# Performance work log

Measured on AMD Instinct MI355X. Metric: run time of the kernel, lower is better.

## Reference

```python
import jax, jax.numpy as jnp
import numpy as np

NUM_BINS_X = 512
NUM_BINS_Y = 512
XL, YL, XH, YH = 0.0, 0.0, 1.0, 1.0
ROUTING_H = 50000.0
ROUTING_V = 50000.0
MACRO_UTIL_H = 10.0
MACRO_UTIL_V = 10.0
NUM_NETS = 131072
PINS_PER_NET = 4
NUM_MOVABLE = 50000
NUM_TERMINALS = 5000
NUM_NODES = NUM_MOVABLE + NUM_TERMINALS
NUM_PINS = NUM_NETS * PINS_PER_NET
BIN_SIZE_X = (XH - XL) / NUM_BINS_X
BIN_SIZE_Y = (YH - YL) / NUM_BINS_Y


def setup_inputs():
    key = jax.random.key(0)
    k1, k2, k3, k4 = jax.random.split(key, 4)
    # pin_pos = [x_0..x_P-1, y_0..y_P-1], pos = [x_0..x_N-1, y_0..y_N-1]
    pin_pos = jax.random.uniform(k1, (2 * NUM_PINS,), dtype=jnp.float32, minval=XL, maxval=XH)
    pos = jax.random.uniform(k2, (2 * NUM_NODES,), dtype=jnp.float32, minval=XL, maxval=0.9 * (XH - XL))
    node_size_x = jax.random.uniform(k3, (NUM_NODES,), dtype=jnp.float32, minval=0.01, maxval=0.05)
    node_size_y = jax.random.uniform(k4, (NUM_NODES,), dtype=jnp.float32, minval=0.01, maxval=0.05)
    net_weights = jnp.ones((NUM_NETS,), jnp.float32)
    rng = np.random.default_rng(0)
    flat_netpin = jnp.asarray(rng.permutation(NUM_PINS).astype(np.int32))
    movable = rng.choice(NUM_MOVABLE, 64, replace=False)
    fixed = NUM_MOVABLE + rng.choice(NUM_TERMINALS, 32, replace=False)
    macro_indexes = jnp.asarray(np.concatenate([movable, fixed]).astype(np.int32))
    return dict(pos=pos, pin_pos=pin_pos, node_size_x=node_size_x, node_size_y=node_size_y,
                net_weights=net_weights, flat_netpin=flat_netpin, macro_indexes=macro_indexes)


def _bin_overlap(lo, hi, origin, bin_size, num_bins):
    # [N, num_bins]: overlap length of interval [lo, hi] with each bin along one axis
    edges = origin + bin_size * jnp.arange(num_bins, dtype=lo.dtype)
    return jnp.clip(jnp.minimum(hi[:, None], edges[None, :] + bin_size)
                    - jnp.maximum(lo[:, None], edges[None, :]), 0.0, None)


def _blur3(m, sigma):
    # torchvision GaussianBlur(kernel_size=3, sigma), separable, reflect padding
    x = jnp.array([-1.0, 0.0, 1.0], m.dtype)
    k = jnp.exp(-0.5 * (x / sigma) ** 2)
    k = k / k.sum()
    mp = jnp.pad(m, ((1, 1), (0, 0)), mode='reflect')
    m = k[0] * mp[:-2] + k[1] * mp[1:-1] + k[2] * mp[2:]
    mp = jnp.pad(m, ((0, 0), (1, 1)), mode='reflect')
    return k[0] * mp[:, :-2] + k[1] * mp[:, 1:-1] + k[2] * mp[:, 2:]


def _rudy_maps(pos, pin_pos, node_size_x, node_size_y, net_weights, flat_netpin, macro_indexes):
    # net bounding boxes from pins (fixed PINS_PER_NET pins per net)
    px = pin_pos[:NUM_PINS][flat_netpin].reshape(NUM_NETS, PINS_PER_NET)
    py = pin_pos[NUM_PINS:][flat_netpin].reshape(NUM_NETS, PINS_PER_NET)
    x_min, x_max = px.min(1), px.max(1)
    y_min, y_max = py.min(1), py.max(1)
    ox = _bin_overlap(x_min, x_max, XL, BIN_SIZE_X, NUM_BINS_X)   # [N, Bx]
    oy = _bin_overlap(y_min, y_max, YL, BIN_SIZE_Y, NUM_BINS_Y)   # [N, By]
    wh = net_weights / (y_max - y_min)  # RUDY horizontal demand density
    wv = net_weights / (x_max - x_min)  # RUDY vertical demand density
    H = jnp.einsum('nx,ny->xy', ox * wh[:, None], oy)
    V = jnp.einsum('nx,ny->xy', ox * wv[:, None], oy)
    # macro contributions
    mx = pos[macro_indexes]
    my = pos[NUM_NODES + macro_indexes]
    msx = node_size_x[macro_indexes]
    msy = node_size_y[macro_indexes]
    area = msx * msy
    mox = _bin_overlap(mx, mx + msx, XL, BIN_SIZE_X, NUM_BINS_X)
    moy = _bin_overlap(my, my + msy, YL, BIN_SIZE_Y, NUM_BINS_Y)
    H = H + jnp.einsum('mx,my->xy', mox * (MACRO_UTIL_H / area)[:, None], moy)
    V = V + jnp.einsum('mx,my->xy', mox * (MACRO_UTIL_V / area)[:, None], moy)
    num_bins = NUM_BINS_X * NUM_BINS_Y
    H = H / (ROUTING_H / num_bins)
    V = V / (ROUTING_V / num_bins)
    sigma = min((XH - XL) / BIN_SIZE_X, (YH - YL) / BIN_SIZE_Y) / 16.0
    return _blur3(H, sigma), _blur3(V, sigma)


def reference(pos, pin_pos, node_size_x, node_size_y, net_weights, flat_netpin, macro_indexes):
    H, V = _rudy_maps(pos, pin_pos, node_size_x, node_size_y, net_weights, flat_netpin, macro_indexes)
    h_ov = jnp.maximum(H - 1.0, 0.0)
    v_ov = jnp.maximum(V - 1.0, 0.0)
    h_cnt = (h_ov > 0).sum()
    v_cnt = (v_ov > 0).sum()
    total_overflow = h_cnt + v_cnt          # total overflow bin area
    max_overflow = jnp.maximum(h_cnt, v_cnt)  # jit-compatible proxy for largest contour area
    route_utilization_map = jnp.maximum(jnp.abs(H), jnp.abs(V))
    return route_utilization_map, max_overflow, total_overflow
```

## Files before the change

kernel.cpp:

```cpp
#include <hip/hip_runtime.h>

#define N_NETS  131072
#define N_PINS  (N_NETS * 4)
#define N_NODES 55000
#define NBBLK   129
#define NPARTS  4
#define CELLCAP 128

__device__ uint4 g_ent[64 * NBBLK * CELLCAP * 2];
__device__ unsigned short g_cellcnt[64 * NBBLK];
__device__ float g_part[NPARTS * 512 * 1024];
__device__ int      g_cnt2[2];
__device__ unsigned g_tick;

__global__ __launch_bounds__(1024) void k_bbox(
    const float* __restrict__ pos, const float* __restrict__ pin_pos,
    const float* __restrict__ nsx, const float* __restrict__ nsy,
    const float* __restrict__ nw,  const int* __restrict__ fnp,
    const int* __restrict__ mid, int nm)
{
    __shared__ int s_cnt[64];
    int tid = threadIdx.x;
    int b = blockIdx.x;
    int t = b * 1024 + tid;
    if (b == 0 && tid == 0) { g_cnt2[0] = 0; g_cnt2[1] = 0; g_tick = 0; }
    if (tid < 64) s_cnt[tid] = 0;
    __syncthreads();

    if (t < N_NETS + nm) {
        float xmin, xmax, ymin, ymax, wh, wv;
        if (t < N_NETS) {
            int4 p = ((const int4*)fnp)[t];
            float x0 = pin_pos[p.x], x1 = pin_pos[p.y], x2 = pin_pos[p.z], x3 = pin_pos[p.w];
            float y0 = pin_pos[N_PINS + p.x], y1 = pin_pos[N_PINS + p.y];
            float y2 = pin_pos[N_PINS + p.z], y3 = pin_pos[N_PINS + p.w];
            xmin = fminf(fminf(x0, x1), fminf(x2, x3));
            xmax = fmaxf(fmaxf(x0, x1), fmaxf(x2, x3));
            ymin = fminf(fminf(y0, y1), fminf(y2, y3));
            ymax = fmaxf(fmaxf(y0, y1), fmaxf(y2, y3));
            float w = nw[t];
            wh = w / (ymax - ymin);
            wv = w / (xmax - xmin);
        } else {
            int idx = mid[t - N_NETS];
            xmin = pos[idx]; ymin = pos[N_NODES + idx];
            float sx = nsx[idx], sy = nsy[idx];
            xmax = xmin + sx; ymax = ymin + sy;
            wh = wv = 10.0f / (sx * sy);
        }
        const float B = 1.0f / 512.0f;
        int xl = min(max((int)(xmin * 512.0f), 0), 511);
        int xh = min(max((int)(xmax * 512.0f), 0), 511);
        int yl = min(max((int)(ymin * 512.0f), 0), 511);
        int yh = min(max((int)(ymax * 512.0f), 0), 511);
        unsigned w0c = (unsigned)yl | ((unsigned)(yl + 1) << 16);
        unsigned w1c = (unsigned)yh | ((unsigned)(yh + 1) << 16);
        float4 pys = make_float4((yl + 1) * B - ymin, ymin - yl * B,
                                 ymax - (yh + 1) * B, yh * B - ymax);
        uint4 Bq = make_uint4(__float_as_uint(pys.x), __float_as_uint(pys.y),
                              __float_as_uint(pys.z), __float_as_uint(pys.w));

        auto put = [&](int row, float px) {
            int s = row & 63;
            int slot = atomicAdd(&s_cnt[s], 1);
            if (slot < CELLCAP) {
                uint4 A;
                A.x = w0c | ((unsigned)(row >> 6) << 29);
                A.y = w1c;
                A.z = __float_as_uint(px * wh);
                A.w = __float_as_uint(px * wv);
                unsigned base = ((unsigned)(s * NBBLK + b) * CELLCAP + (unsigned)slot) * 2u;
                g_ent[base]     = A;
                g_ent[base + 1] = Bq;
            }
        };
        put(xl, (xl + 1) * B - xmin);
        if (xl + 1 < 512) put(xl + 1, xmin - xl * B);
        put(xh, xmax - (xh + 1) * B);
        if (xh + 1 < 512) put(xh + 1, xh * B - xmax);
    }
    __syncthreads();
    if (tid < 64) g_cellcnt[tid * NBBLK + b] = (unsigned short)min(s_cnt[tid], CELLCAP);
}

__global__ __launch_bounds__(1024) void k_deposit() {
    __shared__ float tile[8706];
    __shared__ int s_pref[64];
    __shared__ int s_total;
    int tid = threadIdx.x;
    int s = blockIdx.x >> 2, p = blockIdx.x & 3;
#pragma unroll
    for (int k = tid; k < 8706; k += 1024) tile[k] = 0.0f;

    int lob = (NBBLK * p) >> 2, hib = (NBBLK * (p + 1)) >> 2;
    int nb = hib - lob;
    if (tid < 64) {
        int c = (tid < nb) ? (int)g_cellcnt[s * NBBLK + lob + tid] : 0;
        int v = c;
#pragma unroll
        for (int off = 1; off < 64; off <<= 1) {
            int tv = __shfl_up(v, off);
            if (tid >= off) v += tv;
        }
        s_pref[tid] = v - c;
        if (tid == 63) s_total = v;
    }
    __syncthreads();

    int total = s_total;
    for (int k = tid; k < total; k += 1024) {
        int loJ = 0, hiJ = 63;
#pragma unroll
        for (int st = 0; st < 6; ++st) {
            int mid_ = (loJ + hiJ + 1) >> 1;
            if (s_pref[mid_] <= k) loJ = mid_; else hiJ = mid_ - 1;
        }
        unsigned gidx = ((unsigned)(s * NBBLK + lob + loJ) * CELLCAP
                         + (unsigned)(k - s_pref[loJ])) * 2u;
        uint4 A  = g_ent[gidx];
        uint4 Bq = g_ent[gidx + 1];
        int rr = (int)(A.x >> 29);
        unsigned c0 = A.x & 0xFFFFu, c1 = (A.x >> 16) & 0x1FFFu;
        unsigned c2 = A.y & 0xFFFFu, c3 = A.y >> 16;
        float ah = __uint_as_float(A.z), av = __uint_as_float(A.w);
        float p0 = __uint_as_float(Bq.x), p1 = __uint_as_float(Bq.y);
        float p2 = __uint_as_float(Bq.z), p3 = __uint_as_float(Bq.w);
        int base = rr * 1024;
        int i0 = (c0 < 512u) ? base + 2 * (int)c0 : 8192;
        int i1 = (c1 < 512u) ? base + 2 * (int)c1 : 8192;
        int i2 = (c2 < 512u) ? base + 2 * (int)c2 : 8192;
        int i3 = (c3 < 512u) ? base + 2 * (int)c3 : 8192;
        unsafeAtomicAdd(&tile[i0],     ah * p0);
        unsafeAtomicAdd(&tile[i0 + 1], av * p0);
        unsafeAtomicAdd(&tile[i1],     ah * p1);
        unsafeAtomicAdd(&tile[i1 + 1], av * p1);
        unsafeAtomicAdd(&tile[i2],     ah * p2);
        unsafeAtomicAdd(&tile[i2 + 1], av * p2);
        unsafeAtomicAdd(&tile[i3],     ah * p3);
        unsafeAtomicAdd(&tile[i3 + 1], av * p3);
    }
    __syncthreads();

    int wid = tid >> 6, lane = tid & 63;
    if (wid < 8) {
        float2* rowp = (float2*)&tile[wid * 1024];
        float cx = 0.0f, cy = 0.0f;
        for (int ch = 0; ch < 8; ++ch) {
            float2 v = rowp[ch * 64 + lane];
#pragma unroll
            for (int off = 1; off < 64; off <<= 1) {
                float tx = __shfl_up(v.x, off);
                float ty = __shfl_up(v.y, off);
                if (lane >= off) { v.x += tx; v.y += ty; }
            }
            v.x += cx; v.y += cy;
            rowp[ch * 64 + lane] = v;
            cx = __shfl(v.x, 63); cy = __shfl(v.y, 63);
        }
    }
    __syncthreads();
    int dstp = p * 524288 + (s << 10);
#pragma unroll
    for (int k = 0; k < 8; ++k) {
        int idx = tid + k * 1024;
        int rr = idx >> 10, cc = idx & 1023;
        g_part[dstp + (rr << 16) + cc] = tile[idx];
    }
}

__global__ __launch_bounds__(1024) void k_finish(float* __restrict__ out) {
    __shared__ float sB[16 * 512];
    int tid = threadIdx.x;
    int b = blockIdx.x;
    int lane = tid & 63;
    int c20 = tid & 31;
    int xg = tid >> 5;
    int jj = (c20 < 10) ? c20 : c20 - 10;
    int cy = 8 * b - 1 + jj;
    if (cy < 0) cy = 1;
    if (cy > 511) cy = 510;
    int map = (c20 < 10) ? 0 : 1;
    int gcol = 2 * cy + map;
    const float kw  = expf(-0.5f / 1024.0f);
    const float k1n = 1.0f / (1.0f + 2.0f * kw);
    const float k0n = kw * k1n;
    const float scale = 262144.0f / 50000.0f;
    bool active = c20 < 20;
    int t8  = (c20 < 10) ? c20 - 1 : c20 - 11;

    for (int xo = 0; xo < 16; ++xo) {
        int x = xo * 32 + xg;
        float v = 0.0f;
        if (active) {
            int base = x * 1024 + gcol;
#pragma unroll
            for (int p = 0; p < NPARTS; ++p) v += g_part[p * 524288 + base];
        }
        float vm = __shfl(v, lane - 1);
        float vp = __shfl(v, lane + 1);
        float yb = (k0n * (vm + vp) + k1n * v) * scale;
        if (t8 >= 0 && t8 < 8) sB[(map * 8 + t8) * 512 + x] = yb;
    }
    __syncthreads();

    int w = tid >> 6;
    float s0,s1,s2,s3,s4,s5,s6,s7;
    {
        float4 a  = *(float4*)&sB[w * 512 + lane * 8];
        float4 bq = *(float4*)&sB[w * 512 + lane * 8 + 4];
        s0 = a.x; s1 = s0 + a.y; s2 = s1 + a.z; s3 = s2 + a.w;
        s4 = s3 + bq.x; s5 = s4 + bq.y; s6 = s5 + bq.z; s7 = s6 + bq.w;
        float tot = s7;
#pragma unroll
        for (int off = 1; off < 64; off <<= 1) {
            float tv = __shfl_up(tot, off);
            if (lane >= off) tot += tv;
        }
        float e = tot - s7;
        s0 += e; s1 += e; s2 += e; s3 += e; s4 += e; s5 += e; s6 += e; s7 += e;
    }
    {
        float prev = __shfl(s7, lane - 1);
        float next = __shfl(s0, lane + 1);
        float pm = (lane == 0) ? s1 : prev;
        float nx = (lane == 63) ? s6 : next;
        float b0 = k0n * (pm + s1) + k1n * s0;
        float b1 = k0n * (s0 + s2) + k1n * s1;
        float b2 = k0n * (s1 + s3) + k1n * s2;
        float b3 = k0n * (s2 + s4) + k1n * s3;
        float b4 = k0n * (s3 + s5) + k1n * s4;
        float b5 = k0n * (s4 + s6) + k1n * s5;
        float b6 = k0n * (s5 + s7) + k1n * s6;
        float b7 = k0n * (s6 + nx) + k1n * s7;
        float* row = &sB[w * 512 + lane * 8];
        row[0]=b0; row[1]=b1; row[2]=b2; row[3]=b3;
        row[4]=b4; row[5]=b5; row[6]=b6; row[7]=b7;
    }
    __syncthreads();

    int x = tid >> 1, qh = (tid & 1) * 4;
    float4 o;
    int ch = 0, cv = 0;
#pragma unroll
    for (int k = 0; k < 4; ++k) {
        int tt = qh + k;
        float hv = sB[tt * 512 + x];
        float vv = sB[(8 + tt) * 512 + x];
        ((float*)&o)[k] = fmaxf(fabsf(hv), fabsf(vv));
        ch += (hv > 1.0f); cv += (vv > 1.0f);
    }
    *(float4*)&out[x * 512 + 8 * b + qh] = o;
#pragma unroll
    for (int off = 32; off > 0; off >>= 1) {
        ch += __shfl_down(ch, off);
        cv += __shfl_down(cv, off);
    }
    __shared__ int scnt[2];
    if (tid < 2) scnt[tid] = 0;
    __syncthreads();
    if (lane == 0) { atomicAdd(&scnt[0], ch); atomicAdd(&scnt[1], cv); }
    __syncthreads();
    if (tid == 0) {
        atomicAdd(&g_cnt2[0], scnt[0]);
        atomicAdd(&g_cnt2[1], scnt[1]);
        __threadfence();
        unsigned old = atomicAdd(&g_tick, 1u);
        if ((old & 63u) == 63u) {
            __threadfence();
            int h = atomicAdd(&g_cnt2[0], 0);
            int v = atomicAdd(&g_cnt2[1], 0);
            out[262144] = (float)((h > v) ? h : v);
            out[262145] = (float)(h + v);
        }
    }
}

extern "C" void kernel_launch(void* const* d_in, const int* in_sizes, int n_in,
                              void* d_out, int out_size, void* d_ws, size_t ws_size,
                              hipStream_t stream) {
    const float* pos     = (const float*)d_in[0];
    const float* pin_pos = (const float*)d_in[1];
    const float* nsx     = (const float*)d_in[2];
    const float* nsy     = (const float*)d_in[3];
    const float* nw      = (const float*)d_in[4];
    const int*   fnp     = (const int*)d_in[5];
    const int*   mid     = (const int*)d_in[6];
    int nm = in_sizes[6];
    float* out = (float*)d_out;

    hipLaunchKernelGGL(k_bbox,    dim3(NBBLK), dim3(1024), 0, stream,
                       pos, pin_pos, nsx, nsy, nw, fnp, mid, nm);
    hipLaunchKernelGGL(k_deposit, dim3(256), dim3(1024), 0, stream);
    hipLaunchKernelGGL(k_finish,  dim3(64), dim3(1024), 0, stream, out);
}
```

Before: 66.35 us.

## Rebalance bbox grid to 256 blocks and restructure finish-kernel prefix scan and blur

k_bbox now runs 256 blocks of 512 threads, each looping over 516 nets (RPB), with a smaller per-cell capacity (96). Each deposit partition now reads exactly 64 bbox blocks, so the uneven split is gone. This is meant to spread the scatter over more CUs and cut shared-atomic contention per block. In k_finish, the partition loads are batched four at a time for more memory-level parallelism. The per-lane 8-element scan is replaced by chunked 64-wide wave scans, and the x-direction blur moves into the final output stage, reading neighbours from shared memory. The risk is that a smaller CELLCAP could overflow if the per-block distribution is uneven, and the scan now does more shuffles.

Result: no change. 65.27 us (-1.6%).

```diff
diff --git a/kernel.cpp b/kernel.cpp
--- a/kernel.cpp
+++ b/kernel.cpp
@@ -3,9 +3,10 @@
 #define N_NETS  131072
 #define N_PINS  (N_NETS * 4)
 #define N_NODES 55000
-#define NBBLK   129
+#define NBBLK   256
+#define RPB     516
 #define NPARTS  4
-#define CELLCAP 128
+#define CELLCAP 96
 
 __device__ uint4 g_ent[64 * NBBLK * CELLCAP * 2];
 __device__ unsigned short g_cellcnt[64 * NBBLK];
@@ -13,7 +14,7 @@
 __device__ int      g_cnt2[2];
 __device__ unsigned g_tick;
 
-__global__ __launch_bounds__(1024) void k_bbox(
+__global__ __launch_bounds__(512) void k_bbox(
     const float* __restrict__ pos, const float* __restrict__ pin_pos,
     const float* __restrict__ nsx, const float* __restrict__ nsy,
     const float* __restrict__ nw,  const int* __restrict__ fnp,
@@ -22,12 +23,12 @@
     __shared__ int s_cnt[64];
     int tid = threadIdx.x;
     int b = blockIdx.x;
-    int t = b * 1024 + tid;
     if (b == 0 && tid == 0) { g_cnt2[0] = 0; g_cnt2[1] = 0; g_tick = 0; }
     if (tid < 64) s_cnt[tid] = 0;
     __syncthreads();
 
-    if (t < N_NETS + nm) {
+    int tEnd = min((b + 1) * RPB, N_NETS + nm);
+    for (int t = b * RPB + tid; t < tEnd; t += 512) {
         float xmin, xmax, ymin, ymax, wh, wv;
         if (t < N_NETS) {
             int4 p = ((const int4*)fnp)[t];
@@ -55,10 +56,10 @@
         int yh = min(max((int)(ymax * 512.0f), 0), 511);
         unsigned w0c = (unsigned)yl | ((unsigned)(yl + 1) << 16);
         unsigned w1c = (unsigned)yh | ((unsigned)(yh + 1) << 16);
-        float4 pys = make_float4((yl + 1) * B - ymin, ymin - yl * B,
-                                 ymax - (yh + 1) * B, yh * B - ymax);
-        uint4 Bq = make_uint4(__float_as_uint(pys.x), __float_as_uint(pys.y),
-                              __float_as_uint(pys.z), __float_as_uint(pys.w));
+        uint4 Bq = make_uint4(__float_as_uint((yl + 1) * B - ymin),
+                              __float_as_uint(ymin - yl * B),
+                              __float_as_uint(ymax - (yh + 1) * B),
+                              __float_as_uint(yh * B - ymax));
 
         auto put = [&](int row, float px) {
             int s = row & 63;
@@ -92,10 +93,9 @@
 #pragma unroll
     for (int k = tid; k < 8706; k += 1024) tile[k] = 0.0f;
 
-    int lob = (NBBLK * p) >> 2, hib = (NBBLK * (p + 1)) >> 2;
-    int nb = hib - lob;
+    int lob = p * 64;
     if (tid < 64) {
-        int c = (tid < nb) ? (int)g_cellcnt[s * NBBLK + lob + tid] : 0;
+        int c = (int)g_cellcnt[s * NBBLK + lob + tid];
         int v = c;
 #pragma unroll
         for (int off = 1; off < 64; off <<= 1) {
@@ -170,6 +170,7 @@
 
 __global__ __launch_bounds__(1024) void k_finish(float* __restrict__ out) {
     __shared__ float sB[16 * 512];
+    __shared__ int scnt[2];
     int tid = threadIdx.x;
     int b = blockIdx.x;
     int lane = tid & 63;
@@ -188,77 +189,71 @@
     bool active = c20 < 20;
     int t8  = (c20 < 10) ? c20 - 1 : c20 - 11;
 
-    for (int xo = 0; xo < 16; ++xo) {
-        int x = xo * 32 + xg;
-        float v = 0.0f;
-        if (active) {
-            int base = x * 1024 + gcol;
-#pragma unroll
-            for (int p = 0; p < NPARTS; ++p) v += g_part[p * 524288 + base];
-        }
-        float vm = __shfl(v, lane - 1);
-        float vp = __shfl(v, lane + 1);
-        float yb = (k0n * (vm + vp) + k1n * v) * scale;
-        if (t8 >= 0 && t8 < 8) sB[(map * 8 + t8) * 512 + x] = yb;
-    }
-    __syncthreads();
-
-    int w = tid >> 6;
-    float s0,s1,s2,s3,s4,s5,s6,s7;
+    for (int xo4 = 0; xo4 < 4; ++xo4) {
+        float acc[4];
+#pragma unroll
+        for (int j = 0; j < 4; ++j) {
+            int x = (xo4 * 4 + j) * 32 + xg;
+            float v = 0.0f;
+            if (active) {
+                int base = x * 1024 + gcol;
+#pragma unroll
+                for (int p = 0; p < NPARTS; ++p) v += g_part[p * 524288 + base];
+            }
+            acc[j] = v;
+        }
+#pragma unroll
+        for (int j = 0; j < 4; ++j) {
+            int x = (xo4 * 4 + j) * 32 + xg;
+            float vm = __shfl(acc[j], lane - 1);
+            float vp = __shfl(acc[j], lane + 1);
+            float yb = (k0n * (vm + vp) + k1n * acc[j]) * scale;
+            if (t8 >= 0 && t8 < 8) sB[(map * 8 + t8) * 512 + x] = yb;
+        }
+    }
+    __syncthreads();
+
     {
-        float4 a  = *(float4*)&sB[w * 512 + lane * 8];
-        float4 bq = *(float4*)&sB[w * 512 + lane * 8 + 4];
-        s0 = a.x; s1 = s0 + a.y; s2 = s1 + a.z; s3 = s2 + a.w;
-        s4 = s3 + bq.x; s5 = s4 + bq.y; s6 = s5 + bq.z; s7 = s6 + bq.w;
-        float tot = s7;
-#pragma unroll
-        for (int off = 1; off < 64; off <<= 1) {
-            float tv = __shfl_up(tot, off);
-            if (lane >= off) tot += tv;
-        }
-        float e = tot - s7;
-        s0 += e; s1 += e; s2 += e; s3 += e; s4 += e; s5 += e; s6 += e; s7 += e;
-    }
-    {
-        float prev = __shfl(s7, lane - 1);
-        float next = __shfl(s0, lane + 1);
-        float pm = (lane == 0) ? s1 : prev;
-        float nx = (lane == 63) ? s6 : next;
-        float b0 = k0n * (pm + s1) + k1n * s0;
-        float b1 = k0n * (s0 + s2) + k1n * s1;
-        float b2 = k0n * (s1 + s3) + k1n * s2;
-        float b3 = k0n * (s2 + s4) + k1n * s3;
-        float b4 = k0n * (s3 + s5) + k1n * s4;
-        float b5 = k0n * (s4 + s6) + k1n * s5;
-        float b6 = k0n * (s5 + s7) + k1n * s6;
-        float b7 = k0n * (s6 + nx) + k1n * s7;
-        float* row = &sB[w * 512 + lane * 8];
-        row[0]=b0; row[1]=b1; row[2]=b2; row[3]=b3;
-        row[4]=b4; row[5]=b5; row[6]=b6; row[7]=b7;
+        int w = tid >> 6;
+        float carry = 0.0f;
+        for (int ch = 0; ch < 8; ++ch) {
+            float v = sB[w * 512 + ch * 64 + lane];
+#pragma unroll
+            for (int off = 1; off < 64; off <<= 1) {
+                float tv = __shfl_up(v, off);
+                if (lane >= off) v += tv;
+            }
+            v += carry;
+            sB[w * 512 + ch * 64 + lane] = v;
+            carry = __shfl(v, 63);
+        }
     }
     __syncthreads();
 
     int x = tid >> 1, qh = (tid & 1) * 4;
+    int xm = (x == 0) ? 1 : x - 1;
+    int xp = (x == 511) ? 510 : x + 1;
     float4 o;
-    int ch = 0, cv = 0;
+    int ch_ = 0, cv_ = 0;
 #pragma unroll
     for (int k = 0; k < 4; ++k) {
         int tt = qh + k;
-        float hv = sB[tt * 512 + x];
-        float vv = sB[(8 + tt) * 512 + x];
+        const float* rH = &sB[tt * 512];
+        const float* rV = &sB[(8 + tt) * 512];
+        float hv = k0n * (rH[xm] + rH[xp]) + k1n * rH[x];
+        float vv = k0n * (rV[xm] + rV[xp]) + k1n * rV[x];
         ((float*)&o)[k] = fmaxf(fabsf(hv), fabsf(vv));
-        ch += (hv > 1.0f); cv += (vv > 1.0f);
+        ch_ += (hv > 1.0f); cv_ += (vv > 1.0f);
     }
     *(float4*)&out[x * 512 + 8 * b + qh] = o;
 #pragma unroll
     for (int off = 32; off > 0; off >>= 1) {
-        ch += __shfl_down(ch, off);
-        cv += __shfl_down(cv, off);
-    }
-    __shared__ int scnt[2];
+        ch_ += __shfl_down(ch_, off);
+        cv_ += __shfl_down(cv_, off);
+    }
     if (tid < 2) scnt[tid] = 0;
     __syncthreads();
-    if (lane == 0) { atomicAdd(&scnt[0], ch); atomicAdd(&scnt[1], cv); }
+    if (lane == 0) { atomicAdd(&scnt[0], ch_); atomicAdd(&scnt[1], cv_); }
     __syncthreads();
     if (tid == 0) {
         atomicAdd(&g_cnt2[0], scnt[0]);
@@ -288,7 +283,7 @@
     int nm = in_sizes[6];
     float* out = (float*)d_out;
 
-    hipLaunchKernelGGL(k_bbox,    dim3(NBBLK), dim3(1024), 0, stream,
+    hipLaunchKernelGGL(k_bbox,    dim3(NBBLK), dim3(512), 0, stream,
                        pos, pin_pos, nsx, nsy, nw, fnp, mid, nm);
     hipLaunchKernelGGL(k_deposit, dim3(256), dim3(1024), 0, stream);
     hipLaunchKernelGGL(k_finish,  dim3(64), dim3(1024), 0, stream, out);
```
